# Optimization experiments

Hardware: AMD Instinct MI355X
Metric: run time of the kernel (lower is better)

## Reference

```python
import jax, jax.numpy as jnp
import numpy as np

B, S, D = 4, 2048, 2048


def setup_inputs() -> dict:
    key = jax.random.key(0)
    ks = jax.random.split(key, 24)
    sc = 1.0 / np.sqrt(D)
    def lin(ki, kb):
        W = jax.random.normal(ks[ki], (D, D), dtype=jnp.float32) * sc
        b = jax.random.normal(ks[kb], (D,), dtype=jnp.float32) * 0.01
        return W, b
    Wi, bWi = lin(0, 1); Ui, bUi = lin(2, 3)
    Wf, bWf = lin(4, 5); Uf, bUf = lin(6, 7)
    Wc, bWc = lin(8, 9); Uc, bUc = lin(10, 11)
    Wo, bWo = lin(12, 13); Uo, bUo = lin(14, 15)
    Wp, bp = lin(16, 17)
    x = jax.random.normal(ks[18], (B, S, D), dtype=jnp.float32)
    h = jax.random.normal(ks[19], (B, S, D), dtype=jnp.float32)
    return dict(x=x, h=h, Wi=Wi, bWi=bWi, Ui=Ui, bUi=bUi,
                Wf=Wf, bWf=bWf, Uf=Uf, bUf=bUf,
                Wc=Wc, bWc=bWc, Uc=Uc, bUc=bUc,
                Wo=Wo, bWo=bWo, Uo=Uo, bUo=bUo,
                Wp=Wp, bp=bp)


def reference(x, h, Wi, bWi, Ui, bUi, Wf, bWf, Uf, bUf,
              Wc, bWc, Uc, bUc, Wo, bWo, Uo, bUo, Wp, bp):
    # In the torch source, h[:, t, :] is read BEFORE being overwritten at step t,
    # and c is zero-initialized with each slot written once (so f * c_prev == 0).
    # Hence the computation is exactly parallel over the time axis.
    Zi = jnp.einsum('bsd,ed->bse', x, Wi) + bWi + jnp.einsum('bsd,ed->bse', h, Ui) + bUi
    Zf = jnp.einsum('bsd,ed->bse', x, Wf) + bWf + jnp.einsum('bsd,ed->bse', h, Uf) + bUf
    Zc = jnp.einsum('bsd,ed->bse', x, Wc) + bWc + jnp.einsum('bsd,ed->bse', h, Uc) + bUc
    Zo = jnp.einsum('bsd,ed->bse', x, Wo) + bWo + jnp.einsum('bsd,ed->bse', h, Uo) + bUo
    i = jnp.exp(Zi)
    f = jnp.exp(Zf)  # multiplies a zero cell state in the source; kept for fidelity
    c = f * jnp.zeros_like(f) + i * jnp.tanh(Zc)
    h_out = jax.nn.sigmoid(Zo) * jnp.tanh(c)
    hidden_state = h_out[:, -1, :] @ Wp.T + bp
    return (hidden_state, c)
```

## Files before the change

kernel.cpp:

```cpp
#include <hip/hip_runtime.h>
#include <hip/hip_bf16.h>

typedef short short8 __attribute__((ext_vector_type(8)));
typedef unsigned short ushort8v __attribute__((ext_vector_type(8)));
typedef float f32x4 __attribute__((ext_vector_type(4)));

#define D_DIM 2048
#define KTOT 4096
#define M_TOT 8192
#define NPACK 4096


__device__ __forceinline__ unsigned short f2bf(float f) {
    union { float f; unsigned u; } c; c.f = f;
    unsigned u = c.u;
    u += 0x7fffu + ((u >> 16) & 1u);
    return (unsigned short)(u >> 16);
}

__device__ __forceinline__ float fast_tanh(float x) {
    float ax = fabsf(x);
    float ez = __expf(2.0f * fminf(ax, 15.0f));
    float t = (ez - 1.0f) / (ez + 1.0f);
    return copysignf(t, x);
}

#define GLOAD_LDS16(g, l)                                                     \
    __builtin_amdgcn_global_load_lds(                                         \
        (const __attribute__((address_space(1))) void*)(g),                   \
        (__attribute__((address_space(3))) void*)(l), 16, 0, 0)

#define WAITVM_(N) asm volatile("s_waitcnt vmcnt(" #N ")" ::: "memory")
#define WAITVM(N)  WAITVM_(N)
#define WAITLG_(N) asm volatile("s_waitcnt lgkmcnt(" #N ")" ::: "memory")
#define WAITLG(N)  WAITLG_(N)
#define BAR        __builtin_amdgcn_s_barrier()
#define SCHB       __builtin_amdgcn_sched_barrier(0)
#define PRIO1      __builtin_amdgcn_s_setprio(1)
#define PRIO0      __builtin_amdgcn_s_setprio(0)


__global__ __launch_bounds__(256)
void pack2(const float* __restrict__ X, const float* __restrict__ H,
           __hip_bfloat16* __restrict__ dst, int total8) {
    int t = blockIdx.x * 256 + threadIdx.x;
    if (t >= total8) return;
    long e0 = (long)t * 8;
    long r  = e0 >> 12;
    int  k  = (int)(e0 & 4095);
    const float* src = (k < D_DIM) ? (X + r * D_DIM + k)
                                   : (H + r * D_DIM + (k - D_DIM));
    float4 v0 = *(const float4*)(src);
    float4 v1 = *(const float4*)(src + 4);
    ushort8v o;
    o[0] = f2bf(v0.x); o[1] = f2bf(v0.y); o[2] = f2bf(v0.z); o[3] = f2bf(v0.w);
    o[4] = f2bf(v1.x); o[5] = f2bf(v1.y); o[6] = f2bf(v1.z); o[7] = f2bf(v1.w);
    *(ushort8v*)(dst + e0) = o;
}


__global__ __launch_bounds__(256)
void pack_gates(const float* __restrict__ Wi, const float* __restrict__ Ui,
                const float* __restrict__ Wc, const float* __restrict__ Uc,
                __hip_bfloat16* __restrict__ dst) {
    int t = blockIdx.x * 256 + threadIdx.x;
    const int g = t >> 9;
    const int k = (t & 511) * 8;
    const int w = g & 31;
    const int n = ((g >> 5) << 4) | (w & 15);
    const float* Wm = (w & 16) ? Wc : Wi;
    const float* Um = (w & 16) ? Uc : Ui;
    const float* src = (k < D_DIM) ? (Wm + (size_t)n * D_DIM + k)
                                   : (Um + (size_t)n * D_DIM + (k - D_DIM));
    float4 v0 = *(const float4*)(src);
    float4 v1 = *(const float4*)(src + 4);
    ushort8v o;
    o[0] = f2bf(v0.x); o[1] = f2bf(v0.y); o[2] = f2bf(v0.z); o[3] = f2bf(v0.w);
    o[4] = f2bf(v1.x); o[5] = f2bf(v1.y); o[6] = f2bf(v1.z); o[7] = f2bf(v1.w);
    *(ushort8v*)(dst + (size_t)g * KTOT + k) = o;
}


__device__ __forceinline__ f32x4 mf(short8 a, short8 b, f32x4 c) {
    return __builtin_amdgcn_mfma_f32_16x16x32_bf16(a, b, c, 0, 0, 0);
}

#define RD4A(BUF, IMM)                                                        \
  { _Pragma("unroll") for (int m_ = 0; m_ < 4; ++m_) {                        \
      ak0[m_] = *(const short8*)(rdA0 + (BUF) + (IMM) + m_ * 2048);           \
      ak1[m_] = *(const short8*)(rdA1 + (BUF) + (IMM) + m_ * 2048); } }

#define RDB(d0, d1, BUF, IMM)                                                 \
  { _Pragma("unroll") for (int n_ = 0; n_ < 2; ++n_) {                        \
      d0[n_] = *(const short8*)(rdB0 + (BUF) + (IMM) + n_ * 2048);            \
      d1[n_] = *(const short8*)(rdB1 + (BUF) + (IMM) + n_ * 2048); } }

#define MF16(MB, NB, bk0, bk1)                                                \
  { _Pragma("unroll") for (int m_ = 0; m_ < 4; ++m_)                          \
    _Pragma("unroll") for (int n_ = 0; n_ < 2; ++n_)                          \
      acc[(MB)+m_][(NB)+n_] = mf(ak0[m_], bk0[n_], acc[(MB)+m_][(NB)+n_]);    \
    _Pragma("unroll") for (int m_ = 0; m_ < 4; ++m_)                          \
    _Pragma("unroll") for (int n_ = 0; n_ < 2; ++n_)                          \
      acc[(MB)+m_][(NB)+n_] = mf(ak1[m_], bk1[n_], acc[(MB)+m_][(NB)+n_]); }

#define SA(BUFB, KB) { GLOAD_LDS16(gAh0 + (KB), ldsA + (BUFB) + dOff);        \
                       GLOAD_LDS16(gAh0 + (KB) + 524288, ldsA + (BUFB) + dOff + 8192); \
                       GLOAD_LDS16(gAh1 + (KB), ldsA + (BUFB) + 16384 + dOff); \
                       GLOAD_LDS16(gAh1 + (KB) + 524288, ldsA + (BUFB) + 16384 + dOff + 8192); }
#define SBt(BUFB, KB) { GLOAD_LDS16(gBh0 + (KB), ldsB + (BUFB) + dOff);       \
                        GLOAD_LDS16(gBh0 + (KB) + 524288, ldsB + (BUFB) + dOff + 8192); \
                        GLOAD_LDS16(gBh1 + (KB), ldsB + (BUFB) + 16384 + dOff); \
                        GLOAD_LDS16(gBh1 + (KB) + 524288, ldsB + (BUFB) + 16384 + dOff + 8192); }

#define KTILE(BUF, S_A, S_B, VMN)                                             \
  {                                                                  \
    RD4A(BUF, 0);                                                             \
    RDB(b01k0, b01k1, BUF, 0);                                                \
    RDB(b23k0, b23k1, BUF, 4096);                                             \
    S_A;                                                                      \
    WAITLG(8);                                                                \
    BAR; WAITLG(0); SCHB;                                                     \
    PRIO1; MF16(0, 0, b01k0, b01k1); MF16(0, 2, b23k0, b23k1); PRIO0; BAR;    \
                                                                     \
    RD4A(BUF, 8192);                                                          \
    S_B;                                                                      \
    VMN;                                                                      \
    BAR; WAITLG(0); SCHB;                                                     \
    PRIO1; MF16(4, 0, b01k0, b01k1); MF16(4, 2, b23k0, b23k1); PRIO0; BAR;    \
  }

#define NOSTG (void)0
#define NOVM  (void)0

__global__ __launch_bounds__(512, 2)
void gemm8(const __hip_bfloat16* __restrict__ A,
           const __hip_bfloat16* __restrict__ Bp,
           const float* __restrict__ bWi, const float* __restrict__ bUi,
           const float* __restrict__ bWc, const float* __restrict__ bUc,
           float* __restrict__ Cout) {
    __shared__ __hip_bfloat16 sA[2][2][128][64];
    __shared__ __hip_bfloat16 sB[2][2][128][64];

    const int tid  = threadIdx.x;
    const int wid  = tid >> 6;
    const int lane = tid & 63;

    int bid = blockIdx.x;
    bid = (bid & 7) * 64 + (bid >> 3);
    const int tn = (bid & 15) * 256;
    const int tm = (bid >> 4) * 256;

    const int wr  = (wid >> 2) * 128;
    const int wc  = (wid & 3) * 64;
    const int r15 = lane & 15;
    const int g   = lane >> 4;

    const int sb    = g ^ (r15 & 3);
    const int khb   = (r15 >> 2) & 1;
    const int slot0 = (khb * 4 + sb) * 16;
    const int slot1 = (((1 ^ khb) * 4) + sb) * 16;

    const char* rdA0 = (const char*)sA + (wr >> 7) * 16384 + r15 * 128 + slot0;
    const char* rdA1 = (const char*)sA + (wr >> 7) * 16384 + r15 * 128 + slot1;
    const char* rdB0 = (const char*)sB + (wc >> 7) * 16384 + (wc & 64) * 128 + r15 * 128 + slot0;
    const char* rdB1 = (const char*)sB + (wc >> 7) * 16384 + (wc & 64) * 128 + r15 * 128 + slot1;

    const int r0 = tid >> 3, s0 = tid & 7;
    const int colb = (((s0 >> 2) ^ ((r0 >> 2) & 1)) * 64) +
                     (((s0 & 3) ^ (r0 & 3)) * 16);
    const char* gAh0 = (const char*)(A  + (size_t)(tm + r0) * KTOT) + colb;
    const char* gAh1 = gAh0 + (size_t)128 * KTOT * 2;
    const char* gBh0 = (const char*)(Bp + (size_t)(tn + r0) * KTOT) + colb;
    const char* gBh1 = gBh0 + (size_t)128 * KTOT * 2;
    char* ldsA = (char*)sA;
    char* ldsB = (char*)sB;
    const int dOff = tid * 16;

    f32x4 acc[8][4] = {};
    short8 ak0[4], ak1[4], b01k0[2], b01k1[2], b23k0[2], b23k1[2];

    SA(0, 0);          SBt(0, 0);
    SA(32768, 128);    SBt(32768, 128);
    WAITVM(8);
    BAR;

    KTILE(0, NOSTG, SBt(0, 256), WAITVM(4));

    int kb = 0;
    #pragma unroll 1
    for (int i = 0; i < 30; ++i) {
        KTILE(32768, SA(0, kb + 256),     SBt(32768, kb + 384), WAITVM(4));
        KTILE(0,     SA(32768, kb + 384), SBt(0, kb + 512),     WAITVM(4));
        kb += 256;
    }
    KTILE(32768, SA(0, 7936), SBt(32768, 8064), WAITVM(4));
    KTILE(0,     SA(32768, 8064), NOSTG,        WAITVM(0));
    KTILE(32768, NOSTG, NOSTG, NOVM);

    const int rg4 = (lane >> 4) * 4;
    #pragma unroll
    for (int q = 0; q < 2; ++q) {
        const int gn = (tn >> 1) + (wc >> 1) + q * 16 + r15;
        const float bi_ = bWi[gn] + bUi[gn];
        const float bc_ = bWc[gn] + bUc[gn];
        #pragma unroll
        for (int m = 0; m < 8; ++m) {
            const int gm = tm + wr + m * 16 + rg4;
            #pragma unroll
            for (int r = 0; r < 4; ++r) {
                const float zi = acc[m][2 * q][r]     + bi_;
                const float zc = acc[m][2 * q + 1][r] + bc_;
                Cout[(size_t)(gm + r) * D_DIM + gn] = __expf(zi) * fast_tanh(zc);
            }
        }
    }
}


__global__ __launch_bounds__(256)
void last_gate(const float* __restrict__ x, const float* __restrict__ h,
               const float* __restrict__ Wo, const float* __restrict__ bWo,
               const float* __restrict__ Uo, const float* __restrict__ bUo,
               const float* __restrict__ cfull, float* __restrict__ hbuf) {
    const int o    = blockIdx.x * 4 + (threadIdx.x >> 6);
    const int lane = threadIdx.x & 63;
    const int b = o >> 11, e = o & 2047;
    const float* xr = x  + ((size_t)b * D_DIM + (D_DIM - 1)) * D_DIM;
    const float* hr = h  + ((size_t)b * D_DIM + (D_DIM - 1)) * D_DIM;
    const float* wo = Wo + (size_t)e * D_DIM;
    const float* uo = Uo + (size_t)e * D_DIM;
    float s = 0.0f;
    for (int d = lane; d < D_DIM; d += 64)
        s += xr[d] * wo[d] + hr[d] * uo[d];
    #pragma unroll
    for (int off = 32; off; off >>= 1) s += __shfl_down(s, off);
    if (lane == 0) {
        const float zo  = s + bWo[e] + bUo[e];
        const float sig = 1.0f / (1.0f + __expf(-zo));
        const float cv  = cfull[((size_t)b * D_DIM + (D_DIM - 1)) * D_DIM + e];
        hbuf[o] = sig * fast_tanh(cv);
    }
}


__global__ __launch_bounds__(256)
void proj(const float* __restrict__ hbuf, const float* __restrict__ Wp,
          const float* __restrict__ bp, float* __restrict__ out) {
    const int o    = blockIdx.x * 4 + (threadIdx.x >> 6);
    const int lane = threadIdx.x & 63;
    const int b = o >> 11, p = o & 2047;
    const float* hv = hbuf + (size_t)b * D_DIM;
    const float* wp = Wp   + (size_t)p * D_DIM;
    float s = 0.0f;
    for (int e = lane; e < D_DIM; e += 64)
        s += hv[e] * wp[e];
    #pragma unroll
    for (int off = 32; off; off >>= 1) s += __shfl_down(s, off);
    if (lane == 0) out[o] = s + bp[p];
}


extern "C" void kernel_launch(void* const* d_in, const int* in_sizes, int n_in,
                              void* d_out, int out_size, void* d_ws, size_t ws_size,
                              hipStream_t stream) {
    const float* x   = (const float*)d_in[0];
    const float* h   = (const float*)d_in[1];
    const float* Wi  = (const float*)d_in[2];  const float* bWi = (const float*)d_in[3];
    const float* Ui  = (const float*)d_in[4];  const float* bUi = (const float*)d_in[5];
    const float* Wc  = (const float*)d_in[10]; const float* bWc = (const float*)d_in[11];
    const float* Uc  = (const float*)d_in[12]; const float* bUc = (const float*)d_in[13];
    const float* Wo  = (const float*)d_in[14]; const float* bWo = (const float*)d_in[15];
    const float* Uo  = (const float*)d_in[16]; const float* bUo = (const float*)d_in[17];
    const float* Wp  = (const float*)d_in[18]; const float* bp  = (const float*)d_in[19];

    float* out = (float*)d_out;
    char*  ws  = (char*)d_ws;

    __hip_bfloat16* Abf  = (__hip_bfloat16*)ws;
    __hip_bfloat16* Bpk  = (__hip_bfloat16*)(ws + ((size_t)64 << 20));
    float*          hbuf = (float*)(ws + ((size_t)96 << 20));

    pack2<<<16384, 256, 0, stream>>>(x, h, Abf, M_TOT * KTOT / 8);
    pack_gates<<<8192, 256, 0, stream>>>(Wi, Ui, Wc, Uc, Bpk);

    gemm8<<<(M_TOT / 256) * (NPACK / 256), 512, 0, stream>>>(
        Abf, Bpk, bWi, bUi, bWc, bUc, out + 8192);

    last_gate<<<2048, 256, 0, stream>>>(x, h, Wo, bWo, Uo, bUo, out + 8192,
                                        (float*)hbuf);
    proj<<<2048, 256, 0, stream>>>(hbuf, Wp, bp, out);
}
```

Before: 318.2 us.

## Load B operand fragments directly from global into registers, bypassing LDS

B-matrix tiles now go straight from global memory into per-wave register fragments instead of being staged through shared memory, which halves LDS usage and removes the B LDS reads. The k-loop schedule is reorganised so B loads are issued after the second MFMA half and waited on with separate vmcnt thresholds. The block-index swizzle for L2 locality is also dropped. The cost is that each wave re-fetches its B slice from global/L2 (no sharing across waves in a block), with more global traffic and exposed latency.

Measured after the change: 483.8 us. 52.0% more time.

```diff
diff --git a/kernel.cpp b/kernel.cpp
--- a/kernel.cpp
+++ b/kernel.cpp
@@ -90,47 +90,47 @@
       ak0[m_] = *(const short8*)(rdA0 + (BUF) + (IMM) + m_ * 2048);           \
       ak1[m_] = *(const short8*)(rdA1 + (BUF) + (IMM) + m_ * 2048); } }
 
-#define RDB(d0, d1, BUF, IMM)                                                 \
-  { _Pragma("unroll") for (int n_ = 0; n_ < 2; ++n_) {                        \
-      d0[n_] = *(const short8*)(rdB0 + (BUF) + (IMM) + n_ * 2048);            \
-      d1[n_] = *(const short8*)(rdB1 + (BUF) + (IMM) + n_ * 2048); } }
-
-#define MF16(MB, NB, bk0, bk1)                                                \
+#define LDB(KB)                                                               \
+  { bk0[0] = *(const short8*)(gB0_ + (KB));                                   \
+    bk1[0] = *(const short8*)(gB0_ + (KB) + 64);                              \
+    bk0[1] = *(const short8*)(gB1_ + (KB));                                   \
+    bk1[1] = *(const short8*)(gB1_ + (KB) + 64);                              \
+    bk0[2] = *(const short8*)(gB2_ + (KB));                                   \
+    bk1[2] = *(const short8*)(gB2_ + (KB) + 64);                              \
+    bk0[3] = *(const short8*)(gB3_ + (KB));                                   \
+    bk1[3] = *(const short8*)(gB3_ + (KB) + 64); }
+
+#define MF32(MB)                                                              \
   { _Pragma("unroll") for (int m_ = 0; m_ < 4; ++m_)                          \
-    _Pragma("unroll") for (int n_ = 0; n_ < 2; ++n_)                          \
-      acc[(MB)+m_][(NB)+n_] = mf(ak0[m_], bk0[n_], acc[(MB)+m_][(NB)+n_]);    \
+    _Pragma("unroll") for (int n_ = 0; n_ < 4; ++n_)                          \
+      acc[(MB)+m_][n_] = mf(ak0[m_], bk0[n_], acc[(MB)+m_][n_]);              \
     _Pragma("unroll") for (int m_ = 0; m_ < 4; ++m_)                          \
-    _Pragma("unroll") for (int n_ = 0; n_ < 2; ++n_)                          \
-      acc[(MB)+m_][(NB)+n_] = mf(ak1[m_], bk1[n_], acc[(MB)+m_][(NB)+n_]); }
+    _Pragma("unroll") for (int n_ = 0; n_ < 4; ++n_)                          \
+      acc[(MB)+m_][n_] = mf(ak1[m_], bk1[n_], acc[(MB)+m_][n_]); }
 
 #define SA(BUFB, KB) { GLOAD_LDS16(gAh0 + (KB), ldsA + (BUFB) + dOff);        \
                        GLOAD_LDS16(gAh0 + (KB) + 524288, ldsA + (BUFB) + dOff + 8192); \
                        GLOAD_LDS16(gAh1 + (KB), ldsA + (BUFB) + 16384 + dOff); \
                        GLOAD_LDS16(gAh1 + (KB) + 524288, ldsA + (BUFB) + 16384 + dOff + 8192); }
-#define SBt(BUFB, KB) { GLOAD_LDS16(gBh0 + (KB), ldsB + (BUFB) + dOff);       \
-                        GLOAD_LDS16(gBh0 + (KB) + 524288, ldsB + (BUFB) + dOff + 8192); \
-                        GLOAD_LDS16(gBh1 + (KB), ldsB + (BUFB) + 16384 + dOff); \
-                        GLOAD_LDS16(gBh1 + (KB) + 524288, ldsB + (BUFB) + 16384 + dOff + 8192); }
-
-#define KTILE(BUF, S_A, S_B, VMN)                                             \
+
+#define NOSTG (void)0
+#define NOLDB (void)0
+#define NOVM  (void)0
+
+#define KTILE(BUF, S_A, LB, VMA, VMB)                                         \
   {                                                                  \
     RD4A(BUF, 0);                                                             \
-    RDB(b01k0, b01k1, BUF, 0);                                                \
-    RDB(b23k0, b23k1, BUF, 4096);                                             \
     S_A;                                                                      \
-    WAITLG(8);                                                                \
+    VMA;                                                                      \
     BAR; WAITLG(0); SCHB;                                                     \
-    PRIO1; MF16(0, 0, b01k0, b01k1); MF16(0, 2, b23k0, b23k1); PRIO0; BAR;    \
+    PRIO1; MF32(0); PRIO0; BAR;                                               \
                                                                      \
     RD4A(BUF, 8192);                                                          \
-    S_B;                                                                      \
-    VMN;                                                                      \
     BAR; WAITLG(0); SCHB;                                                     \
-    PRIO1; MF16(4, 0, b01k0, b01k1); MF16(4, 2, b23k0, b23k1); PRIO0; BAR;    \
-  }
-
-#define NOSTG (void)0
-#define NOVM  (void)0
+    PRIO1; MF32(4); PRIO0;                                                    \
+    LB;                                                                       \
+    VMB;                                                                      \
+    BAR; }
 
 __global__ __launch_bounds__(512, 2)
 void gemm8(const __hip_bfloat16* __restrict__ A,
@@ -139,14 +139,12 @@
            const float* __restrict__ bWc, const float* __restrict__ bUc,
            float* __restrict__ Cout) {
     __shared__ __hip_bfloat16 sA[2][2][128][64];
-    __shared__ __hip_bfloat16 sB[2][2][128][64];
 
     const int tid  = threadIdx.x;
     const int wid  = tid >> 6;
     const int lane = tid & 63;
 
-    int bid = blockIdx.x;
-    bid = (bid & 7) * 64 + (bid >> 3);
+    const int bid = blockIdx.x;
     const int tn = (bid & 15) * 256;
     const int tm = (bid >> 4) * 256;
 
@@ -162,40 +160,39 @@
 
     const char* rdA0 = (const char*)sA + (wr >> 7) * 16384 + r15 * 128 + slot0;
     const char* rdA1 = (const char*)sA + (wr >> 7) * 16384 + r15 * 128 + slot1;
-    const char* rdB0 = (const char*)sB + (wc >> 7) * 16384 + (wc & 64) * 128 + r15 * 128 + slot0;
-    const char* rdB1 = (const char*)sB + (wc >> 7) * 16384 + (wc & 64) * 128 + r15 * 128 + slot1;
 
     const int r0 = tid >> 3, s0 = tid & 7;
     const int colb = (((s0 >> 2) ^ ((r0 >> 2) & 1)) * 64) +
                      (((s0 & 3) ^ (r0 & 3)) * 16);
-    const char* gAh0 = (const char*)(A  + (size_t)(tm + r0) * KTOT) + colb;
+    const char* gAh0 = (const char*)(A + (size_t)(tm + r0) * KTOT) + colb;
     const char* gAh1 = gAh0 + (size_t)128 * KTOT * 2;
-    const char* gBh0 = (const char*)(Bp + (size_t)(tn + r0) * KTOT) + colb;
-    const char* gBh1 = gBh0 + (size_t)128 * KTOT * 2;
     char* ldsA = (char*)sA;
-    char* ldsB = (char*)sB;
     const int dOff = tid * 16;
 
+    const char* gB0_ = (const char*)Bp + (size_t)(tn + wc + r15) * (KTOT * 2) + g * 16;
+    const char* gB1_ = gB0_ + 16 * (KTOT * 2);
+    const char* gB2_ = gB0_ + 32 * (KTOT * 2);
+    const char* gB3_ = gB0_ + 48 * (KTOT * 2);
+
     f32x4 acc[8][4] = {};
-    short8 ak0[4], ak1[4], b01k0[2], b01k1[2], b23k0[2], b23k1[2];
-
-    SA(0, 0);          SBt(0, 0);
-    SA(32768, 128);    SBt(32768, 128);
-    WAITVM(8);
+    short8 ak0[4], ak1[4], bk0[4], bk1[4];
+
+    SA(0, 0);
+    LDB(0);
+    SA(32768, 128);
+    WAITVM(4);
     BAR;
 
-    KTILE(0, NOSTG, SBt(0, 256), WAITVM(4));
+    KTILE(0, NOSTG, LDB(128), WAITVM(4), WAITVM(8));
 
     int kb = 0;
     #pragma unroll 1
-    for (int i = 0; i < 30; ++i) {
-        KTILE(32768, SA(0, kb + 256),     SBt(32768, kb + 384), WAITVM(4));
-        KTILE(0,     SA(32768, kb + 384), SBt(0, kb + 512),     WAITVM(4));
+    for (int i = 0; i < 31; ++i) {
+        KTILE(32768, SA(0, kb + 256),     LDB(kb + 256), WAITVM(4), WAITVM(8));
+        KTILE(0,     SA(32768, kb + 384), LDB(kb + 384), WAITVM(4), WAITVM(8));
         kb += 256;
     }
-    KTILE(32768, SA(0, 7936), SBt(32768, 8064), WAITVM(4));
-    KTILE(0,     SA(32768, 8064), NOSTG,        WAITVM(0));
-    KTILE(32768, NOSTG, NOSTG, NOVM);
+    KTILE(32768, NOSTG, NOLDB, WAITVM(0), NOVM);
 
     const int rg4 = (lane >> 4) * 4;
     #pragma unroll
```

## Switch gate GEMM to 32x32x16 bf16 MFMA with matching LDS swizzle and packing

Applied to the files above, without the earlier changes.

Replaces the 16x16x32 MFMA tiles with 32x32x16 bf16 MFMA, so each wave computes 4x2 32x32 fragments instead of 8x4 16x16 fragments. The weight packing is regrouped into 32-column interleaved i/c blocks so each 32-wide N fragment holds only one gate. The LDS swizzle and the global-to-LDS column mapping become a simple 8-way XOR, and the epilogue is rewritten for the 32x32 accumulator layout. The aim is fewer LDS fragment reads per MFMA flop and higher MFMA throughput per instruction, at the cost of larger accumulators and a riskier new swizzle and epilogue index mapping.

New measurement: 348.6 us. 9.5% more time.

```diff
diff --git a/kernel.cpp b/kernel.cpp
--- a/kernel.cpp
+++ b/kernel.cpp
@@ -3,7 +3,7 @@
 
 typedef short short8 __attribute__((ext_vector_type(8)));
 typedef unsigned short ushort8v __attribute__((ext_vector_type(8)));
-typedef float f32x4 __attribute__((ext_vector_type(4)));
+typedef float f32x16 __attribute__((ext_vector_type(16)));
 
 #define D_DIM 2048
 #define KTOT 4096
@@ -66,10 +66,10 @@
     int t = blockIdx.x * 256 + threadIdx.x;
     const int g = t >> 9;
     const int k = (t & 511) * 8;
-    const int w = g & 31;
-    const int n = ((g >> 5) << 4) | (w & 15);
-    const float* Wm = (w & 16) ? Wc : Wi;
-    const float* Um = (w & 16) ? Uc : Ui;
+    const int w = g & 63;
+    const int n = ((g >> 6) << 5) | (w & 31);
+    const float* Wm = (w & 32) ? Wc : Wi;
+    const float* Um = (w & 32) ? Uc : Ui;
     const float* src = (k < D_DIM) ? (Wm + (size_t)n * D_DIM + k)
                                    : (Um + (size_t)n * D_DIM + (k - D_DIM));
     float4 v0 = *(const float4*)(src);
@@ -81,27 +81,26 @@
 }
 
 
-__device__ __forceinline__ f32x4 mf(short8 a, short8 b, f32x4 c) {
-    return __builtin_amdgcn_mfma_f32_16x16x32_bf16(a, b, c, 0, 0, 0);
-}
-
-#define RD4A(BUF, IMM)                                                        \
-  { _Pragma("unroll") for (int m_ = 0; m_ < 4; ++m_) {                        \
-      ak0[m_] = *(const short8*)(rdA0 + (BUF) + (IMM) + m_ * 2048);           \
-      ak1[m_] = *(const short8*)(rdA1 + (BUF) + (IMM) + m_ * 2048); } }
-
-#define RDB(d0, d1, BUF, IMM)                                                 \
-  { _Pragma("unroll") for (int n_ = 0; n_ < 2; ++n_) {                        \
-      d0[n_] = *(const short8*)(rdB0 + (BUF) + (IMM) + n_ * 2048);            \
-      d1[n_] = *(const short8*)(rdB1 + (BUF) + (IMM) + n_ * 2048); } }
-
-#define MF16(MB, NB, bk0, bk1)                                                \
-  { _Pragma("unroll") for (int m_ = 0; m_ < 4; ++m_)                          \
+__device__ __forceinline__ f32x16 mf32(short8 a, short8 b, f32x16 c) {
+    return __builtin_amdgcn_mfma_f32_32x32x16_bf16(a, b, c, 0, 0, 0);
+}
+
+#define RDA(dst, BUF, MF)                                                     \
+  { dst[0] = *(const short8*)(rdAk0 + (BUF) + (MF) * 4096);                   \
+    dst[1] = *(const short8*)(rdAk1 + (BUF) + (MF) * 4096);                   \
+    dst[2] = *(const short8*)(rdAk2 + (BUF) + (MF) * 4096);                   \
+    dst[3] = *(const short8*)(rdAk3 + (BUF) + (MF) * 4096); }
+#define RDBn(dst, BUF, NF)                                                    \
+  { dst[0] = *(const short8*)(rdBk0 + (BUF) + (NF) * 4096);                   \
+    dst[1] = *(const short8*)(rdBk1 + (BUF) + (NF) * 4096);                   \
+    dst[2] = *(const short8*)(rdBk2 + (BUF) + (NF) * 4096);                   \
+    dst[3] = *(const short8*)(rdBk3 + (BUF) + (NF) * 4096); }
+
+#define MF16Q(MB)                                                             \
+  { _Pragma("unroll") for (int ks = 0; ks < 4; ++ks)                          \
+    _Pragma("unroll") for (int m_ = 0; m_ < 2; ++m_)                          \
     _Pragma("unroll") for (int n_ = 0; n_ < 2; ++n_)                          \
-      acc[(MB)+m_][(NB)+n_] = mf(ak0[m_], bk0[n_], acc[(MB)+m_][(NB)+n_]);    \
-    _Pragma("unroll") for (int m_ = 0; m_ < 4; ++m_)                          \
-    _Pragma("unroll") for (int n_ = 0; n_ < 2; ++n_)                          \
-      acc[(MB)+m_][(NB)+n_] = mf(ak1[m_], bk1[n_], acc[(MB)+m_][(NB)+n_]); }
+      acc[(MB)+m_][n_] = mf32(aa[m_][ks], bk[n_][ks], acc[(MB)+m_][n_]); }
 
 #define SA(BUFB, KB) { GLOAD_LDS16(gAh0 + (KB), ldsA + (BUFB) + dOff);        \
                        GLOAD_LDS16(gAh0 + (KB) + 524288, ldsA + (BUFB) + dOff + 8192); \
@@ -112,25 +111,23 @@
                         GLOAD_LDS16(gBh1 + (KB), ldsB + (BUFB) + 16384 + dOff); \
                         GLOAD_LDS16(gBh1 + (KB) + 524288, ldsB + (BUFB) + 16384 + dOff + 8192); }
 
+#define NOSTG (void)0
+#define NOVM  (void)0
+
 #define KTILE(BUF, S_A, S_B, VMN)                                             \
-  {                                                                  \
-    RD4A(BUF, 0);                                                             \
-    RDB(b01k0, b01k1, BUF, 0);                                                \
-    RDB(b23k0, b23k1, BUF, 4096);                                             \
+  {           \
+    RDA(aa[0], BUF, 0); RDA(aa[1], BUF, 1);                                   \
+    RDBn(bk[0], BUF, 0); RDBn(bk[1], BUF, 1);                                 \
     S_A;                                                                      \
     WAITLG(8);                                                                \
     BAR; WAITLG(0); SCHB;                                                     \
-    PRIO1; MF16(0, 0, b01k0, b01k1); MF16(0, 2, b23k0, b23k1); PRIO0; BAR;    \
-                                                                     \
-    RD4A(BUF, 8192);                                                          \
+    PRIO1; MF16Q(0); PRIO0; BAR;                                              \
+                                 \
+    RDA(aa[0], BUF, 2); RDA(aa[1], BUF, 3);                                   \
     S_B;                                                                      \
     VMN;                                                                      \
     BAR; WAITLG(0); SCHB;                                                     \
-    PRIO1; MF16(4, 0, b01k0, b01k1); MF16(4, 2, b23k0, b23k1); PRIO0; BAR;    \
-  }
-
-#define NOSTG (void)0
-#define NOVM  (void)0
+    PRIO1; MF16Q(2); PRIO0; BAR; }
 
 __global__ __launch_bounds__(512, 2)
 void gemm8(const __hip_bfloat16* __restrict__ A,
@@ -152,22 +149,23 @@
 
     const int wr  = (wid >> 2) * 128;
     const int wc  = (wid & 3) * 64;
-    const int r15 = lane & 15;
-    const int g   = lane >> 4;
-
-    const int sb    = g ^ (r15 & 3);
-    const int khb   = (r15 >> 2) & 1;
-    const int slot0 = (khb * 4 + sb) * 16;
-    const int slot1 = (((1 ^ khb) * 4) + sb) * 16;
-
-    const char* rdA0 = (const char*)sA + (wr >> 7) * 16384 + r15 * 128 + slot0;
-    const char* rdA1 = (const char*)sA + (wr >> 7) * 16384 + r15 * 128 + slot1;
-    const char* rdB0 = (const char*)sB + (wc >> 7) * 16384 + (wc & 64) * 128 + r15 * 128 + slot0;
-    const char* rdB1 = (const char*)sB + (wc >> 7) * 16384 + (wc & 64) * 128 + r15 * 128 + slot1;
+    const int r31 = lane & 31;
+    const int h   = lane >> 5;
+
+    const int r7 = r31 & 7;
+    const char* rdAb = (const char*)sA + (wr >> 7) * 16384 + r31 * 128;
+    const char* rdAk0 = rdAb + (((0 + h) ^ r7) * 16);
+    const char* rdAk1 = rdAb + (((2 + h) ^ r7) * 16);
+    const char* rdAk2 = rdAb + (((4 + h) ^ r7) * 16);
+    const char* rdAk3 = rdAb + (((6 + h) ^ r7) * 16);
+    const char* rdBb = (const char*)sB + (wc >> 7) * 16384 + (wc & 64) * 128 + r31 * 128;
+    const char* rdBk0 = rdBb + (((0 + h) ^ r7) * 16);
+    const char* rdBk1 = rdBb + (((2 + h) ^ r7) * 16);
+    const char* rdBk2 = rdBb + (((4 + h) ^ r7) * 16);
+    const char* rdBk3 = rdBb + (((6 + h) ^ r7) * 16);
 
     const int r0 = tid >> 3, s0 = tid & 7;
-    const int colb = (((s0 >> 2) ^ ((r0 >> 2) & 1)) * 64) +
-                     (((s0 & 3) ^ (r0 & 3)) * 16);
+    const int colb = ((s0 ^ (r0 & 7)) * 16);
     const char* gAh0 = (const char*)(A  + (size_t)(tm + r0) * KTOT) + colb;
     const char* gAh1 = gAh0 + (size_t)128 * KTOT * 2;
     const char* gBh0 = (const char*)(Bp + (size_t)(tn + r0) * KTOT) + colb;
@@ -176,8 +174,8 @@
     char* ldsB = (char*)sB;
     const int dOff = tid * 16;
 
-    f32x4 acc[8][4] = {};
-    short8 ak0[4], ak1[4], b01k0[2], b01k1[2], b23k0[2], b23k1[2];
+    f32x16 acc[4][2] = {};
+    short8 aa[2][4], bk[2][4];
 
     SA(0, 0);          SBt(0, 0);
     SA(32768, 128);    SBt(32768, 128);
@@ -197,21 +195,17 @@
     KTILE(0,     SA(32768, 8064), NOSTG,        WAITVM(0));
     KTILE(32768, NOSTG, NOSTG, NOVM);
 
-    const int rg4 = (lane >> 4) * 4;
+    const int gn = ((tn + wc) >> 1) + r31;
+    const float bi_ = bWi[gn] + bUi[gn];
+    const float bc_ = bWc[gn] + bUc[gn];
     #pragma unroll
-    for (int q = 0; q < 2; ++q) {
-        const int gn = (tn >> 1) + (wc >> 1) + q * 16 + r15;
-        const float bi_ = bWi[gn] + bUi[gn];
-        const float bc_ = bWc[gn] + bUc[gn];
+    for (int mf = 0; mf < 4; ++mf) {
         #pragma unroll
-        for (int m = 0; m < 8; ++m) {
-            const int gm = tm + wr + m * 16 + rg4;
-            #pragma unroll
-            for (int r = 0; r < 4; ++r) {
-                const float zi = acc[m][2 * q][r]     + bi_;
-                const float zc = acc[m][2 * q + 1][r] + bc_;
-                Cout[(size_t)(gm + r) * D_DIM + gn] = __expf(zi) * fast_tanh(zc);
-            }
+        for (int rg = 0; rg < 16; ++rg) {
+            const int gm = tm + wr + mf * 32 + (rg & 3) + 8 * (rg >> 2) + 4 * h;
+            const float zi = acc[mf][0][rg] + bi_;
+            const float zc = acc[mf][1][rg] + bc_;
+            Cout[(size_t)gm * D_DIM + gn] = __expf(zi) * fast_tanh(zc);
         }
     }
 }
```

## Prefetch both A halves per k-tile and drop intermediate barriers

Applied to the files above, without the earlier changes.

The k-tile loop now loads both halves of the A fragments from LDS into separate register sets up front. It issues the second global-to-LDS stage earlier and runs the two MFMA groups back to back with a single trailing barrier, instead of two barrier pairs per tile. The MFMA loop order is also changed to reuse each A fragment across all four B columns. The aim is fewer barriers and more overlap of LDS reads with MFMA work, at the cost of extra VGPRs for the second A fragment set, which could hurt occupancy at 512 threads and 2 blocks per CU. Whether the earlier S_B issue is still safe for buffer reuse depends on the barrier placement.

Measured after the change: 350.7 us. +10.2%, slower.

```diff
diff --git a/kernel.cpp b/kernel.cpp
--- a/kernel.cpp
+++ b/kernel.cpp
@@ -85,23 +85,25 @@
     return __builtin_amdgcn_mfma_f32_16x16x32_bf16(a, b, c, 0, 0, 0);
 }
 
-#define RD4A(BUF, IMM)                                                        \
+#define RD4A(D0, D1, BUF, IMM)                                                \
   { _Pragma("unroll") for (int m_ = 0; m_ < 4; ++m_) {                        \
-      ak0[m_] = *(const short8*)(rdA0 + (BUF) + (IMM) + m_ * 2048);           \
-      ak1[m_] = *(const short8*)(rdA1 + (BUF) + (IMM) + m_ * 2048); } }
+      D0[m_] = *(const short8*)(rdA0 + (BUF) + (IMM) + m_ * 2048);            \
+      D1[m_] = *(const short8*)(rdA1 + (BUF) + (IMM) + m_ * 2048); } }
 
 #define RDB(d0, d1, BUF, IMM)                                                 \
   { _Pragma("unroll") for (int n_ = 0; n_ < 2; ++n_) {                        \
       d0[n_] = *(const short8*)(rdB0 + (BUF) + (IMM) + n_ * 2048);            \
       d1[n_] = *(const short8*)(rdB1 + (BUF) + (IMM) + n_ * 2048); } }
 
-#define MF16(MB, NB, bk0, bk1)                                                \
+#define MF32(A0, A1, MB)                                                      \
   { _Pragma("unroll") for (int m_ = 0; m_ < 4; ++m_)                          \
-    _Pragma("unroll") for (int n_ = 0; n_ < 2; ++n_)                          \
-      acc[(MB)+m_][(NB)+n_] = mf(ak0[m_], bk0[n_], acc[(MB)+m_][(NB)+n_]);    \
+    _Pragma("unroll") for (int n_ = 0; n_ < 2; ++n_) {                        \
+      acc[(MB)+m_][n_]   = mf(A0[m_], b01k0[n_], acc[(MB)+m_][n_]);           \
+      acc[(MB)+m_][2+n_] = mf(A0[m_], b23k0[n_], acc[(MB)+m_][2+n_]); }       \
     _Pragma("unroll") for (int m_ = 0; m_ < 4; ++m_)                          \
-    _Pragma("unroll") for (int n_ = 0; n_ < 2; ++n_)                          \
-      acc[(MB)+m_][(NB)+n_] = mf(ak1[m_], bk1[n_], acc[(MB)+m_][(NB)+n_]); }
+    _Pragma("unroll") for (int n_ = 0; n_ < 2; ++n_) {                        \
+      acc[(MB)+m_][n_]   = mf(A1[m_], b01k1[n_], acc[(MB)+m_][n_]);           \
+      acc[(MB)+m_][2+n_] = mf(A1[m_], b23k1[n_], acc[(MB)+m_][2+n_]); } }
 
 #define SA(BUFB, KB) { GLOAD_LDS16(gAh0 + (KB), ldsA + (BUFB) + dOff);        \
                        GLOAD_LDS16(gAh0 + (KB) + 524288, ldsA + (BUFB) + dOff + 8192); \
@@ -112,25 +114,26 @@
                         GLOAD_LDS16(gBh1 + (KB), ldsB + (BUFB) + 16384 + dOff); \
                         GLOAD_LDS16(gBh1 + (KB) + 524288, ldsB + (BUFB) + 16384 + dOff + 8192); }
 
-#define KTILE(BUF, S_A, S_B, VMN)                                             \
-  {                                                                  \
-    RD4A(BUF, 0);                                                             \
-    RDB(b01k0, b01k1, BUF, 0);                                                \
-    RDB(b23k0, b23k1, BUF, 4096);                                             \
-    S_A;                                                                      \
-    WAITLG(8);                                                                \
-    BAR; WAITLG(0); SCHB;                                                     \
-    PRIO1; MF16(0, 0, b01k0, b01k1); MF16(0, 2, b23k0, b23k1); PRIO0; BAR;    \
-                                                                     \
-    RD4A(BUF, 8192);                                                          \
-    S_B;                                                                      \
-    VMN;                                                                      \
-    BAR; WAITLG(0); SCHB;                                                     \
-    PRIO1; MF16(4, 0, b01k0, b01k1); MF16(4, 2, b23k0, b23k1); PRIO0; BAR;    \
-  }
-
 #define NOSTG (void)0
 #define NOVM  (void)0
+
+#define KTILE(BUF, S_A, S_B, VMN)                                             \
+  { RDB(b01k0, b01k1, BUF, 0);                                                \
+    RDB(b23k0, b23k1, BUF, 4096);                                             \
+    RD4A(ak0, ak1, BUF, 0);                                                   \
+    S_A;                                                                      \
+    WAITLG(8);                         \
+    BAR;                                     \
+    S_B;                                                                      \
+    RD4A(akb0, akb1, BUF, 8192);                    \
+    WAITLG(8);                                 \
+    SCHB;                                                                     \
+    PRIO1; MF32(ak0, ak1, 0); PRIO0;                                          \
+    WAITLG(0);                          \
+    SCHB;                                                                     \
+    PRIO1; MF32(akb0, akb1, 4); PRIO0;                                        \
+    VMN;                                                                      \
+    BAR; }
 
 __global__ __launch_bounds__(512, 2)
 void gemm8(const __hip_bfloat16* __restrict__ A,
@@ -177,7 +180,8 @@
     const int dOff = tid * 16;
 
     f32x4 acc[8][4] = {};
-    short8 ak0[4], ak1[4], b01k0[2], b01k1[2], b23k0[2], b23k1[2];
+    short8 ak0[4], ak1[4], akb0[4], akb1[4];
+    short8 b01k0[2], b01k1[2], b23k0[2], b23k1[2];
 
     SA(0, 0);          SBt(0, 0);
     SA(32768, 128);    SBt(32768, 128);
```
